# Optimization experiments

Measured on AMD Instinct MI355X. Metric: run time of the kernel, lower is better.

The kernel has to match this reference:

```python
import jax, jax.numpy as jnp
import numpy as np

D = 512
SCALE = 1.0 / np.sqrt(D).astype(np.float32)


def setup_inputs() -> dict:
    key = jax.random.key(0)
    ks = jax.random.split(key, 6)
    B, S = 8, 2048
    x = jax.random.normal(ks[0], (B, S, D), dtype=jnp.float32)
    bias = jax.random.normal(ks[1], (1,), dtype=jnp.float32)
    key_padding_mask = jax.random.randint(ks[2], (B, S), 0, 2).astype(jnp.bool_)
    # nn.Linear weights, stored as [out, in]; y = x @ W.T
    Wq = jax.random.normal(ks[3], (D, D), dtype=jnp.float32) * (1.0 / np.sqrt(D))
    Wk = jax.random.normal(ks[4], (D, D), dtype=jnp.float32) * (1.0 / np.sqrt(D))
    Wv = jax.random.normal(ks[5], (D, D), dtype=jnp.float32) * (1.0 / np.sqrt(D))
    return {"x": x, "bias": bias, "key_padding_mask": key_padding_mask,
            "Wq": Wq, "Wk": Wk, "Wv": Wv}


def reference(x, bias, key_padding_mask, Wq, Wk, Wv):
    # Projections (Linear without bias): [B,S,D] @ [D,D]^T
    Q = jnp.einsum('bsd,ed->bse', x, Wq)
    K = jnp.einsum('bsd,ed->bse', x, Wk)
    V = jnp.einsum('bsd,ed->bse', x, Wv)
    # Scaled scores with additive scalar bias: [B,S,S]
    scores = jnp.einsum('bqd,bkd->bqk', Q, K) * SCALE + bias
    # Key padding mask: mask keys (last dim) with -inf
    scores = jnp.where(key_padding_mask[:, None, :], -jnp.inf, scores)
    attn = jax.nn.softmax(scores, axis=-1)
    attn = jnp.nan_to_num(attn, nan=0.0)  # fully-masked rows -> 0
    # Dropout is inference no-op
    return jnp.einsum('bqk,bkd->bqd', attn, V)
```

## Files before the change

### kernel.cpp

```cpp
#include <hip/hip_runtime.h>

typedef short bf16x8 __attribute__((ext_vector_type(8)));
typedef float f32x4 __attribute__((ext_vector_type(4)));
typedef float f32x16 __attribute__((ext_vector_type(16)));

__device__ __forceinline__ ushort f2bf(float f) {
    union { float f; unsigned u; } v; v.f = f;
    unsigned r = (v.u + 0x7fffu + ((v.u >> 16) & 1u)) >> 16;
    return (ushort)r;
}
__device__ __forceinline__ float bf2f(ushort u) {
    union { unsigned u; float f; } v; v.u = ((unsigned)u) << 16;
    return v.f;
}
__device__ __forceinline__ void async_copy16(void* lds, const void* g) {
    __builtin_amdgcn_global_load_lds(
        (const __attribute__((address_space(1))) unsigned*)g,
        (__attribute__((address_space(3))) unsigned*)lds, 16, 0, 0);
}
__device__ __forceinline__ void lds_barrier() {
    asm volatile("s_waitcnt lgkmcnt(0)\n\ts_barrier" ::: "memory");
}

__global__ __launch_bounds__(256)
void prep_kernel(const float* __restrict__ x, const float* __restrict__ Wq,
                 const float* __restrict__ Wk, const float* __restrict__ Wv,
                 const int* __restrict__ mask,
                 ushort* __restrict__ xb, ushort* __restrict__ wqT,
                 ushort* __restrict__ wkT, ushort* __restrict__ wvb,
                 int* __restrict__ idx, int* __restrict__ cnt)
{
    const int bid = blockIdx.x, t = threadIdx.x;
    if (bid < 8192) {
        int i = (bid * 256 + t) * 4;
        float4 v = *(const float4*)(x + i);
        ushort4 o;
        o.x = f2bf(v.x); o.y = f2bf(v.y); o.z = f2bf(v.z); o.w = f2bf(v.w);
        *(ushort4*)(xb + i) = o;
    } else if (bid < 8320) {
        __shared__ ushort T[64][72];
        int r = bid - 8192;
        const int z = r >> 6; r &= 63;
        const float* in = z ? Wk : Wq;
        ushort* out     = z ? wkT : wqT;
        const int r0 = (r >> 3) * 64, c0 = (r & 7) * 64;
        const int rr = t >> 3, cc8 = (t & 7) * 8;
        #pragma unroll
        for (int pass = 0; pass < 2; ++pass) {
            int rw = rr + pass * 32;
            float4 a = *(const float4*)(in + (size_t)(r0 + rw) * 512 + c0 + cc8);
            float4 bq = *(const float4*)(in + (size_t)(r0 + rw) * 512 + c0 + cc8 + 4);
            T[rw][cc8+0]=f2bf(a.x);  T[rw][cc8+1]=f2bf(a.y);  T[rw][cc8+2]=f2bf(a.z);  T[rw][cc8+3]=f2bf(a.w);
            T[rw][cc8+4]=f2bf(bq.x); T[rw][cc8+5]=f2bf(bq.y); T[rw][cc8+6]=f2bf(bq.z); T[rw][cc8+7]=f2bf(bq.w);
        }
        __syncthreads();
        const int c = t >> 2, seg = (t & 3) * 16;
        ushort tmp[16];
        #pragma unroll
        for (int j = 0; j < 16; ++j) tmp[j] = T[seg + j][c];
        *(uint4*)(out + (size_t)(c0 + c) * 512 + r0 + seg)     = *(uint4*)&tmp[0];
        *(uint4*)(out + (size_t)(c0 + c) * 512 + r0 + seg + 8) = *(uint4*)&tmp[8];
    } else if (bid < 8576) {
        int i = ((bid - 8320) * 256 + t) * 4;
        float4 v = *(const float4*)(Wv + i);
        ushort4 o;
        o.x = f2bf(v.x); o.y = f2bf(v.y); o.z = f2bf(v.z); o.w = f2bf(v.w);
        *(ushort4*)(wvb + i) = o;
    } else {
        __shared__ int sc[256];
        int seg = bid - 8576, b = seg >> 1, half = seg & 1;
        const int* m = mask + b * 2048 + half * 1024;
        int v0 = (m[t*4+0] == 0), v1 = (m[t*4+1] == 0);
        int v2 = (m[t*4+2] == 0), v3 = (m[t*4+3] == 0);
        int c = v0 + v1 + v2 + v3;
        sc[t] = c; __syncthreads();
        for (int ofs = 1; ofs < 256; ofs <<= 1) {
            int xx = (t >= ofs) ? sc[t - ofs] : 0;
            __syncthreads(); sc[t] += xx; __syncthreads();
        }
        int pos = sc[t] - c + seg * 1024;
        if (v0) idx[pos++] = t*4+0;
        if (v1) idx[pos++] = t*4+1;
        if (v2) idx[pos++] = t*4+2;
        if (v3) idx[pos++] = t*4+3;
        if (t == 255) cnt[seg] = sc[255];
    }
}

__device__ __forceinline__ int map_row(const int* __restrict__ idx,
                                       const int* __restrict__ cnt, int row) {
    int seg = row >> 10, j = row & 1023;
    int src = (j < cnt[seg]) ? idx[(seg << 10) + j] : 0;
    return (seg << 10) + src;
}

__device__ __forceinline__ void gemm_core(const ushort* __restrict__ A,
                                          const ushort* __restrict__ B,
                                          ushort* __restrict__ C,
                                          int N, int K, int mBase, int nBase,
                                          int mapA, int mapB,
                                          const int* __restrict__ idx,
                                          const int* __restrict__ cnt)
{
    __shared__ ushort As[128][32];
    __shared__ ushort Bs[128][32];
    const int tid = threadIdx.x;
    const int lane = tid & 63, wave = tid >> 6;
    const int wm = wave >> 1, wn = wave & 1;
    const int lr = lane & 15, lq = lane >> 4;
    const int sr = lane >> 2;
    const int sc = (lane & 3) * 8;

    const ushort* aptr[2];
    const ushort* bptr[2];
    #pragma unroll
    for (int j = 0; j < 2; ++j) {
        int ra = mBase + wave * 32 + j * 16 + sr;
        int rb = nBase + wave * 32 + j * 16 + sr;
        int sa = mapA ? map_row(idx, cnt, ra) : ra;
        int sb = mapB ? map_row(idx, cnt, rb) : rb;
        aptr[j] = A + (size_t)sa * K + sc;
        bptr[j] = B + (size_t)sb * K + sc;
    }

    f32x4 acc[4][4];
    #pragma unroll
    for (int i = 0; i < 4; ++i)
        #pragma unroll
        for (int j = 0; j < 4; ++j) acc[i][j] = (f32x4){0.f, 0.f, 0.f, 0.f};

    for (int k0 = 0; k0 < K; k0 += 32) {
        __syncthreads();
        #pragma unroll
        for (int j = 0; j < 2; ++j) {
            int rbase = wave * 32 + j * 16;
            async_copy16(&As[rbase][0], aptr[j] + k0);
            async_copy16(&Bs[rbase][0], bptr[j] + k0);
        }
        __syncthreads();
        bf16x8 af[4], bfr[4];
        #pragma unroll
        for (int mi = 0; mi < 4; ++mi) af[mi] = *(const bf16x8*)&As[wm * 64 + mi * 16 + lr][lq * 8];
        #pragma unroll
        for (int ni = 0; ni < 4; ++ni) bfr[ni] = *(const bf16x8*)&Bs[wn * 64 + ni * 16 + lr][lq * 8];
        #pragma unroll
        for (int mi = 0; mi < 4; ++mi)
            #pragma unroll
            for (int ni = 0; ni < 4; ++ni)
                acc[mi][ni] = __builtin_amdgcn_mfma_f32_16x16x32_bf16(af[mi], bfr[ni], acc[mi][ni], 0, 0, 0);
    }
    #pragma unroll
    for (int mi = 0; mi < 4; ++mi)
        #pragma unroll
        for (int ni = 0; ni < 4; ++ni)
            #pragma unroll
            for (int r = 0; r < 4; ++r) {
                int m = mBase + wm * 64 + mi * 16 + lq * 4 + r;
                int n = nBase + wn * 64 + ni * 16 + lr;
                C[(size_t)m * N + n] = f2bf(acc[mi][ni][r]);
            }
}

__global__ __launch_bounds__(256, 2)
void gemm_m(const ushort* __restrict__ A, const ushort* __restrict__ B,
            ushort* __restrict__ C) {
    gemm_core(A, B, C, 512, 512, blockIdx.y * 128, blockIdx.x * 128,
              0, 0, nullptr, nullptr);
}

__global__ __launch_bounds__(256, 2)
void gemm_kv(const ushort* __restrict__ xb, const ushort* __restrict__ Mb,
             ushort* __restrict__ Kc, const ushort* __restrict__ wv,
             ushort* __restrict__ Vtc, const int* __restrict__ idx,
             const int* __restrict__ cnt)
{
    if (blockIdx.z == 0) {
        int mBase = blockIdx.y * 128, nBase = blockIdx.x * 128;
        if ((mBase & 1023) >= cnt[mBase >> 10]) return;
        gemm_core(xb, Mb, Kc, 512, 512, mBase, nBase, 1, 0, idx, cnt);
    } else {
        int mBase = blockIdx.x * 128, nBase = blockIdx.y * 128;
        if ((nBase & 1023) >= cnt[nBase >> 10]) return;
        gemm_core(wv, xb, Vtc, 16384, 512, mBase, nBase, 0, 1, idx, cnt);
    }
}

__global__ __launch_bounds__(256, 2)
void attn_kernel(const ushort* __restrict__ Qg, const ushort* __restrict__ Kcg,
                 const ushort* __restrict__ Vtcg, const int* __restrict__ cntg,
                 ushort* __restrict__ Pog, float* __restrict__ Mlg)
{
    const int S = 2048;
    const float SL2E = 0.0637587160f;

    __shared__ ushort Ks[32][548];
    __shared__ ushort Vs[512][36];
    __shared__ ushort Ps[2][32][36];

    const int lin = blockIdx.x + 32 * blockIdx.y + 256 * blockIdx.z;
    const int seg = (lin & 7) * 2 + (lin >> 8);
    const int qt  = (lin >> 3) & 31;
    const int b = seg >> 1, half = seg & 1;

    const int tid = threadIdx.x, lane = tid & 63, wave = tid >> 6;
    const int lr = lane & 15, lq = lane >> 4;
    const int p = wave >> 1, s = wave & 1;
    const int l32 = lane & 31, lh = lane >> 5;

    const int n = cntg[seg];
    const int ntiles = (n + 31) >> 5;

    const ushort* Qp = Qg + ((size_t)b * S + qt * 64 + wave * 16 + lr) * 512;
    bf16x8 qf[16];
    #pragma unroll
    for (int c = 0; c < 16; ++c) qf[c] = *(const bf16x8*)(Qp + c * 32 + lq * 8);

    f32x16 o[8];
    #pragma unroll
    for (int i = 0; i < 8; ++i)
        #pragma unroll
        for (int r = 0; r < 16; ++r) o[i][r] = 0.f;
    float l_i[4] = {0.f, 0.f, 0.f, 0.f};

    const char* Kseg = (const char*)(Kcg + (size_t)seg * 1024 * 512);
    const char* Vseg = (const char*)Vtcg + (size_t)(seg * 1024) * 2;

    {
        #pragma unroll
        for (int i = 0; i < 8; ++i) {
            int row = wave * 8 + i;
            async_copy16(&Ks[row][0], Kseg + (size_t)row * 1024 + lane * 16);
        }
    }

    for (int kt = 0; kt < ntiles; ++kt) {
        const int key0 = kt * 32;
        __syncthreads();
        uint4 vreg[8];
        {
            const char* gV = Vseg + (size_t)key0 * 2;
            #pragma unroll
            for (int i = 0; i < 8; ++i) {
                int off = i * 4096 + tid * 16;
                vreg[i] = *(const uint4*)(gV + (size_t)(off >> 6) * 32768 + (off & 63));
            }
        }
        const bool va0 = (key0 + lr) < n;
        const bool va1 = (key0 + 16 + lr) < n;
        f32x4 sA = (f32x4){0.f,0.f,0.f,0.f}, sB = (f32x4){0.f,0.f,0.f,0.f};
        f32x4 sC = (f32x4){0.f,0.f,0.f,0.f}, sD = (f32x4){0.f,0.f,0.f,0.f};
        __builtin_amdgcn_s_setprio(1);
        #pragma unroll
        for (int ks = 0; ks < 16; ks += 2) {
            bf16x8 kf0a = *(const bf16x8*)&Ks[lr][ks * 32 + lq * 8];
            bf16x8 kf1a = *(const bf16x8*)&Ks[16 + lr][ks * 32 + lq * 8];
            bf16x8 kf0b = *(const bf16x8*)&Ks[lr][(ks + 1) * 32 + lq * 8];
            bf16x8 kf1b = *(const bf16x8*)&Ks[16 + lr][(ks + 1) * 32 + lq * 8];
            sA = __builtin_amdgcn_mfma_f32_16x16x32_bf16(qf[ks], kf0a, sA, 0, 0, 0);
            sB = __builtin_amdgcn_mfma_f32_16x16x32_bf16(qf[ks], kf1a, sB, 0, 0, 0);
            sC = __builtin_amdgcn_mfma_f32_16x16x32_bf16(qf[ks + 1], kf0b, sC, 0, 0, 0);
            sD = __builtin_amdgcn_mfma_f32_16x16x32_bf16(qf[ks + 1], kf1b, sD, 0, 0, 0);
        }
        __builtin_amdgcn_s_setprio(0);
        #pragma unroll
        for (int r = 0; r < 4; ++r) {
            float s0 = sA[r] + sC[r], s1 = sB[r] + sD[r];
            float p0 = va0 ? exp2f(fmaf(s0, SL2E, -8.f)) : 0.f;
            float p1 = va1 ? exp2f(fmaf(s1, SL2E, -8.f)) : 0.f;
            l_i[r] += p0 + p1;
            Ps[p][16 * s + lq * 4 + r][lr]      = f2bf(p0);
            Ps[p][16 * s + lq * 4 + r][16 + lr] = f2bf(p1);
        }
        #pragma unroll
        for (int i = 0; i < 8; ++i) {
            int off = i * 4096 + tid * 16;
            int row = off >> 6, col = off & 63;
            *(uint4*)((char*)Vs + row * 72 + col) = vreg[i];
        }
        lds_barrier();
        if (kt + 1 < ntiles) {
            const char* gK = Kseg + (size_t)(key0 + 32) * 1024;
            #pragma unroll
            for (int i = 0; i < 8; ++i) {
                int row = wave * 8 + i;
                async_copy16(&Ks[row][0], gK + (size_t)row * 1024 + lane * 16);
            }
        }
        bf16x8 pA0 = *(const bf16x8*)&Ps[p][l32][lh * 8];
        bf16x8 pA1 = *(const bf16x8*)&Ps[p][l32][16 + lh * 8];
        __builtin_amdgcn_s_setprio(1);
        #pragma unroll
        for (int dt = 0; dt < 8; ++dt) {
            int d = s * 256 + dt * 32 + l32;
            bf16x8 v0 = *(const bf16x8*)&Vs[d][lh * 8];
            bf16x8 v1 = *(const bf16x8*)&Vs[d][16 + lh * 8];
            o[dt] = __builtin_amdgcn_mfma_f32_32x32x16_bf16(pA0, v0, o[dt], 0, 0, 0);
            o[dt] = __builtin_amdgcn_mfma_f32_32x32x16_bf16(pA1, v1, o[dt], 0, 0, 0);
        }
        __builtin_amdgcn_s_setprio(0);
    }
    #pragma unroll
    for (int r = 0; r < 4; ++r)
        #pragma unroll
        for (int off = 1; off < 16; off <<= 1)
            l_i[r] += __shfl_xor(l_i[r], off, 16);
    const size_t growbase = (size_t)half * 16384 + (size_t)b * S + qt * 64;
    if (lr == 0) {
        #pragma unroll
        for (int r = 0; r < 4; ++r)
            Mlg[growbase + wave * 16 + lq * 4 + r] = l_i[r];
    }
    ushort* Pop = Pog + (growbase + p * 32) * 512;
    #pragma unroll
    for (int dt = 0; dt < 8; ++dt) {
        int ocol = s * 256 + dt * 32 + l32;
        #pragma unroll
        for (int r = 0; r < 16; ++r) {
            int orow = (r & 3) + 8 * (r >> 2) + 4 * lh;
            Pop[(size_t)orow * 512 + ocol] = f2bf(o[dt][r]);
        }
    }
}

__global__ __launch_bounds__(256)
void combine_kernel(const ushort* __restrict__ Po, const float* __restrict__ Ml,
                    float* __restrict__ out)
{
    int i = (blockIdx.x * 256 + threadIdx.x) * 4;
    int row = i >> 9;
    float l = Ml[row] + Ml[16384 + row];
    float s = l > 0.f ? 1.f / l : 0.f;
    ushort4 p1 = *(const ushort4*)(Po + i);
    ushort4 p2 = *(const ushort4*)(Po + 8388608 + i);
    float4 o;
    o.x = (bf2f(p1.x) + bf2f(p2.x)) * s;
    o.y = (bf2f(p1.y) + bf2f(p2.y)) * s;
    o.z = (bf2f(p1.z) + bf2f(p2.z)) * s;
    o.w = (bf2f(p1.w) + bf2f(p2.w)) * s;
    *(float4*)(out + i) = o;
}

extern "C" void kernel_launch(void* const* d_in, const int* in_sizes, int n_in,
                              void* d_out, int out_size, void* d_ws, size_t ws_size,
                              hipStream_t stream) {
    const float* x  = (const float*)d_in[0];
    const int* mask = (const int*)d_in[2];
    const float* Wq = (const float*)d_in[3];
    const float* Wk = (const float*)d_in[4];
    const float* Wv = (const float*)d_in[5];
    float* out = (float*)d_out;

    ushort* ws   = (ushort*)d_ws;
    ushort* xb   = ws;
    ushort* wqT  = ws + 8388608;
    ushort* wkT  = wqT + 262144;
    ushort* wvb  = wkT + 262144;
    ushort* Pob  = ws + 9175040;
    ushort* Mb   = ws + 17563648;
    int*    idxb = (int*)(ws + 17825792);
    ushort* Kc   = ws + 25952256;
    ushort* Vtc  = ws + 34340864;
    float*  Mlb  = (float*)(ws + 42729472);
    int*    cntb = (int*)(ws + 42795008);

    prep_kernel<<<8592, 256, 0, stream>>>(x, Wq, Wk, Wv, mask,
                                          xb, wqT, wkT, wvb, idxb, cntb);
    gemm_m<<<dim3(4, 4), 256, 0, stream>>>(wqT, wkT, Mb);
    gemm_kv<<<dim3(4, 128, 2), 256, 0, stream>>>(xb, Mb, Kc, wvb, Vtc, idxb, cntb);
    attn_kernel<<<dim3(32, 8, 2), 256, 0, stream>>>(xb, Kc, Vtc, cntb, Pob, Mlb);
    combine_kernel<<<8192, 256, 0, stream>>>(Pob, Mlb, out);
}
```

Before: 214.2 us.

## Write V in MFMA-fragment tiled layout and load V directly from global

The V projection epilogue now writes V^T into a layout pre-tiled to match the 32x32x16 MFMA B-operand fragments. The attention kernel then reads V fragments straight from global memory (L2) and drops the Vs LDS staging buffer with its register round-trip. This removes LDS writes and reads for V and frees shared memory, which may allow higher occupancy. In exchange the V loads now sit on the MFMA critical path with global latency, and the K prefetch is issued later in the loop.

```diff
diff --git a/kernel.cpp b/kernel.cpp
--- a/kernel.cpp
+++ b/kernel.cpp
@@ -100,7 +100,8 @@
                                           int N, int K, int mBase, int nBase,
                                           int mapA, int mapB,
                                           const int* __restrict__ idx,
-                                          const int* __restrict__ cnt)
+                                          const int* __restrict__ cnt,
+                                          int vt)
 {
     __shared__ ushort As[128][32];
     __shared__ ushort Bs[128][32];
@@ -157,7 +158,16 @@
             for (int r = 0; r < 4; ++r) {
                 int m = mBase + wm * 64 + mi * 16 + lq * 4 + r;
                 int n = nBase + wn * 64 + ni * 16 + lr;
-                C[(size_t)m * N + n] = f2bf(acc[mi][ni][r]);
+                float val = acc[mi][ni][r];
+                if (!vt) {
+                    C[(size_t)m * N + n] = f2bf(val);
+                } else {
+                    int sseg = n >> 10, key = n & 1023;
+                    size_t ix = (size_t)sseg * 524288 + (size_t)(key >> 5) * 16384
+                              + (size_t)(m >> 5) * 1024 + ((key >> 4) & 1) * 512
+                              + (m & 31) * 16 + (key & 15);
+                    C[ix] = f2bf(val);
+                }
             }
 }
 
@@ -165,7 +175,7 @@
 void gemm_m(const ushort* __restrict__ A, const ushort* __restrict__ B,
             ushort* __restrict__ C) {
     gemm_core(A, B, C, 512, 512, blockIdx.y * 128, blockIdx.x * 128,
-              0, 0, nullptr, nullptr);
+              0, 0, nullptr, nullptr, 0);
 }
 
 __global__ __launch_bounds__(256, 2)
@@ -177,11 +187,11 @@
     if (blockIdx.z == 0) {
         int mBase = blockIdx.y * 128, nBase = blockIdx.x * 128;
         if ((mBase & 1023) >= cnt[mBase >> 10]) return;
-        gemm_core(xb, Mb, Kc, 512, 512, mBase, nBase, 1, 0, idx, cnt);
+        gemm_core(xb, Mb, Kc, 512, 512, mBase, nBase, 1, 0, idx, cnt, 0);
     } else {
         int mBase = blockIdx.x * 128, nBase = blockIdx.y * 128;
         if ((nBase & 1023) >= cnt[nBase >> 10]) return;
-        gemm_core(wv, xb, Vtc, 16384, 512, mBase, nBase, 0, 1, idx, cnt);
+        gemm_core(wv, xb, Vtc, 16384, 512, mBase, nBase, 0, 1, idx, cnt, 1);
     }
 }
 
@@ -194,7 +204,6 @@
     const float SL2E = 0.0637587160f;
 
     __shared__ ushort Ks[32][548];
-    __shared__ ushort Vs[512][36];
     __shared__ ushort Ps[2][32][36];
 
     const int lin = blockIdx.x + 32 * blockIdx.y + 256 * blockIdx.z;
@@ -223,7 +232,7 @@
     float l_i[4] = {0.f, 0.f, 0.f, 0.f};
 
     const char* Kseg = (const char*)(Kcg + (size_t)seg * 1024 * 512);
-    const char* Vseg = (const char*)Vtcg + (size_t)(seg * 1024) * 2;
+    const ushort* Vseg = Vtcg + (size_t)seg * 524288;
 
     {
         #pragma unroll
@@ -236,15 +245,6 @@
     for (int kt = 0; kt < ntiles; ++kt) {
         const int key0 = kt * 32;
         __syncthreads();
-        uint4 vreg[8];
-        {
-            const char* gV = Vseg + (size_t)key0 * 2;
-            #pragma unroll
-            for (int i = 0; i < 8; ++i) {
-                int off = i * 4096 + tid * 16;
-                vreg[i] = *(const uint4*)(gV + (size_t)(off >> 6) * 32768 + (off & 63));
-            }
-        }
         const bool va0 = (key0 + lr) < n;
         const bool va1 = (key0 + 16 + lr) < n;
         f32x4 sA = (f32x4){0.f,0.f,0.f,0.f}, sB = (f32x4){0.f,0.f,0.f,0.f};
@@ -271,13 +271,20 @@
             Ps[p][16 * s + lq * 4 + r][lr]      = f2bf(p0);
             Ps[p][16 * s + lq * 4 + r][16 + lr] = f2bf(p1);
         }
-        #pragma unroll
-        for (int i = 0; i < 8; ++i) {
-            int off = i * 4096 + tid * 16;
-            int row = off >> 6, col = off & 63;
-            *(uint4*)((char*)Vs + row * 72 + col) = vreg[i];
-        }
         lds_barrier();
+        bf16x8 pA0 = *(const bf16x8*)&Ps[p][l32][lh * 8];
+        bf16x8 pA1 = *(const bf16x8*)&Ps[p][l32][16 + lh * 8];
+        const ushort* Vt = Vseg + (size_t)kt * 16384 + l32 * 16 + lh * 8;
+        __builtin_amdgcn_s_setprio(1);
+        #pragma unroll
+        for (int dt = 0; dt < 8; ++dt) {
+            const int db = s * 8 + dt;
+            bf16x8 v0 = *(const bf16x8*)(Vt + db * 1024);
+            bf16x8 v1 = *(const bf16x8*)(Vt + db * 1024 + 512);
+            o[dt] = __builtin_amdgcn_mfma_f32_32x32x16_bf16(pA0, v0, o[dt], 0, 0, 0);
+            o[dt] = __builtin_amdgcn_mfma_f32_32x32x16_bf16(pA1, v1, o[dt], 0, 0, 0);
+        }
+        __builtin_amdgcn_s_setprio(0);
         if (kt + 1 < ntiles) {
             const char* gK = Kseg + (size_t)(key0 + 32) * 1024;
             #pragma unroll
@@ -286,18 +293,6 @@
                 async_copy16(&Ks[row][0], gK + (size_t)row * 1024 + lane * 16);
             }
         }
-        bf16x8 pA0 = *(const bf16x8*)&Ps[p][l32][lh * 8];
-        bf16x8 pA1 = *(const bf16x8*)&Ps[p][l32][16 + lh * 8];
-        __builtin_amdgcn_s_setprio(1);
-        #pragma unroll
-        for (int dt = 0; dt < 8; ++dt) {
-            int d = s * 256 + dt * 32 + l32;
-            bf16x8 v0 = *(const bf16x8*)&Vs[d][lh * 8];
-            bf16x8 v1 = *(const bf16x8*)&Vs[d][16 + lh * 8];
-            o[dt] = __builtin_amdgcn_mfma_f32_32x32x16_bf16(pA0, v0, o[dt], 0, 0, 0);
-            o[dt] = __builtin_amdgcn_mfma_f32_32x32x16_bf16(pA1, v1, o[dt], 0, 0, 0);
-        }
-        __builtin_amdgcn_s_setprio(0);
     }
     #pragma unroll
     for (int r = 0; r < 4; ++r)
```

Result: slower. 250.8 us (+17.1%).

## Fuse Wq^T·Wk product GEMM into prep kernel and widen combine vectors

Applied to the files above, without the earlier changes.

Drops the separate gemm_m launch and the transposed bf16 copies of Wq and Wk. The M = Wq^T·Wk product is now computed inside the prep kernel by 16 extra blocks that read fp32 weights directly, convert to bf16 and transpose into LDS, then run MFMA. This removes one kernel launch and one round-trip of intermediate weight buffers. The combine kernel also switches to 8 elements per thread with 16-byte loads, halving its grid. The trade-off is that these 16 GEMM blocks run inside the large prep grid with uncoalesced scalar LDS stores and no pipelining, so they may become a tail at the end of prep.

```diff
diff --git a/kernel.cpp b/kernel.cpp
--- a/kernel.cpp
+++ b/kernel.cpp
@@ -3,6 +3,7 @@
 typedef short bf16x8 __attribute__((ext_vector_type(8)));
 typedef float f32x4 __attribute__((ext_vector_type(4)));
 typedef float f32x16 __attribute__((ext_vector_type(16)));
+typedef ushort u16x8 __attribute__((ext_vector_type(8)));
 
 __device__ __forceinline__ ushort f2bf(float f) {
     union { float f; unsigned u; } v; v.f = f;
@@ -26,8 +27,8 @@
 void prep_kernel(const float* __restrict__ x, const float* __restrict__ Wq,
                  const float* __restrict__ Wk, const float* __restrict__ Wv,
                  const int* __restrict__ mask,
-                 ushort* __restrict__ xb, ushort* __restrict__ wqT,
-                 ushort* __restrict__ wkT, ushort* __restrict__ wvb,
+                 ushort* __restrict__ xb, ushort* __restrict__ wvb,
+                 ushort* __restrict__ Mb,
                  int* __restrict__ idx, int* __restrict__ cnt)
 {
     const int bid = blockIdx.x, t = threadIdx.x;
@@ -37,38 +38,72 @@
         ushort4 o;
         o.x = f2bf(v.x); o.y = f2bf(v.y); o.z = f2bf(v.z); o.w = f2bf(v.w);
         *(ushort4*)(xb + i) = o;
-    } else if (bid < 8320) {
-        __shared__ ushort T[64][72];
-        int r = bid - 8192;
-        const int z = r >> 6; r &= 63;
-        const float* in = z ? Wk : Wq;
-        ushort* out     = z ? wkT : wqT;
-        const int r0 = (r >> 3) * 64, c0 = (r & 7) * 64;
-        const int rr = t >> 3, cc8 = (t & 7) * 8;
-        #pragma unroll
-        for (int pass = 0; pass < 2; ++pass) {
-            int rw = rr + pass * 32;
-            float4 a = *(const float4*)(in + (size_t)(r0 + rw) * 512 + c0 + cc8);
-            float4 bq = *(const float4*)(in + (size_t)(r0 + rw) * 512 + c0 + cc8 + 4);
-            T[rw][cc8+0]=f2bf(a.x);  T[rw][cc8+1]=f2bf(a.y);  T[rw][cc8+2]=f2bf(a.z);  T[rw][cc8+3]=f2bf(a.w);
-            T[rw][cc8+4]=f2bf(bq.x); T[rw][cc8+5]=f2bf(bq.y); T[rw][cc8+6]=f2bf(bq.z); T[rw][cc8+7]=f2bf(bq.w);
-        }
-        __syncthreads();
-        const int c = t >> 2, seg = (t & 3) * 16;
-        ushort tmp[16];
-        #pragma unroll
-        for (int j = 0; j < 16; ++j) tmp[j] = T[seg + j][c];
-        *(uint4*)(out + (size_t)(c0 + c) * 512 + r0 + seg)     = *(uint4*)&tmp[0];
-        *(uint4*)(out + (size_t)(c0 + c) * 512 + r0 + seg + 8) = *(uint4*)&tmp[8];
-    } else if (bid < 8576) {
-        int i = ((bid - 8320) * 256 + t) * 4;
+    } else if (bid < 8208) {
+        __shared__ ushort As[128][32];
+        __shared__ ushort Bs[128][32];
+        const int bb = bid - 8192;
+        const int m0 = (bb >> 2) * 128, n0 = (bb & 3) * 128;
+        const int lane = t & 63, wave = t >> 6;
+        const int wm = wave >> 1, wn = wave & 1;
+        const int lr = lane & 15, lq = lane >> 4;
+        const int kk = t >> 3, mm = (t & 7) * 16;
+
+        f32x4 acc[4][4];
+        #pragma unroll
+        for (int i2 = 0; i2 < 4; ++i2)
+            #pragma unroll
+            for (int j2 = 0; j2 < 4; ++j2) acc[i2][j2] = (f32x4){0.f,0.f,0.f,0.f};
+
+        for (int k0 = 0; k0 < 512; k0 += 32) {
+            float4 qa[4], kb[4];
+            #pragma unroll
+            for (int j = 0; j < 4; ++j) {
+                qa[j] = *(const float4*)(Wq + (size_t)(k0 + kk) * 512 + m0 + mm + j * 4);
+                kb[j] = *(const float4*)(Wk + (size_t)(k0 + kk) * 512 + n0 + mm + j * 4);
+            }
+            __syncthreads();
+            #pragma unroll
+            for (int j = 0; j < 4; ++j) {
+                As[mm + j*4 + 0][kk] = f2bf(qa[j].x);
+                As[mm + j*4 + 1][kk] = f2bf(qa[j].y);
+                As[mm + j*4 + 2][kk] = f2bf(qa[j].z);
+                As[mm + j*4 + 3][kk] = f2bf(qa[j].w);
+                Bs[mm + j*4 + 0][kk] = f2bf(kb[j].x);
+                Bs[mm + j*4 + 1][kk] = f2bf(kb[j].y);
+                Bs[mm + j*4 + 2][kk] = f2bf(kb[j].z);
+                Bs[mm + j*4 + 3][kk] = f2bf(kb[j].w);
+            }
+            __syncthreads();
+            bf16x8 af[4], bfr[4];
+            #pragma unroll
+            for (int mi = 0; mi < 4; ++mi) af[mi]  = *(const bf16x8*)&As[wm * 64 + mi * 16 + lr][lq * 8];
+            #pragma unroll
+            for (int ni = 0; ni < 4; ++ni) bfr[ni] = *(const bf16x8*)&Bs[wn * 64 + ni * 16 + lr][lq * 8];
+            #pragma unroll
+            for (int mi = 0; mi < 4; ++mi)
+                #pragma unroll
+                for (int ni = 0; ni < 4; ++ni)
+                    acc[mi][ni] = __builtin_amdgcn_mfma_f32_16x16x32_bf16(af[mi], bfr[ni], acc[mi][ni], 0, 0, 0);
+        }
+        #pragma unroll
+        for (int mi = 0; mi < 4; ++mi)
+            #pragma unroll
+            for (int ni = 0; ni < 4; ++ni)
+                #pragma unroll
+                for (int r = 0; r < 4; ++r) {
+                    int m = m0 + wm * 64 + mi * 16 + lq * 4 + r;
+                    int n = n0 + wn * 64 + ni * 16 + lr;
+                    Mb[(size_t)m * 512 + n] = f2bf(acc[mi][ni][r]);
+                }
+    } else if (bid < 8464) {
+        int i = ((bid - 8208) * 256 + t) * 4;
         float4 v = *(const float4*)(Wv + i);
         ushort4 o;
         o.x = f2bf(v.x); o.y = f2bf(v.y); o.z = f2bf(v.z); o.w = f2bf(v.w);
         *(ushort4*)(wvb + i) = o;
     } else {
         __shared__ int sc[256];
-        int seg = bid - 8576, b = seg >> 1, half = seg & 1;
+        int seg = bid - 8464, b = seg >> 1, half = seg & 1;
         const int* m = mask + b * 2048 + half * 1024;
         int v0 = (m[t*4+0] == 0), v1 = (m[t*4+1] == 0);
         int v2 = (m[t*4+2] == 0), v3 = (m[t*4+3] == 0);
@@ -162,13 +197,6 @@
 }
 
 __global__ __launch_bounds__(256, 2)
-void gemm_m(const ushort* __restrict__ A, const ushort* __restrict__ B,
-            ushort* __restrict__ C) {
-    gemm_core(A, B, C, 512, 512, blockIdx.y * 128, blockIdx.x * 128,
-              0, 0, nullptr, nullptr);
-}
-
-__global__ __launch_bounds__(256, 2)
 void gemm_kv(const ushort* __restrict__ xb, const ushort* __restrict__ Mb,
              ushort* __restrict__ Kc, const ushort* __restrict__ wv,
              ushort* __restrict__ Vtc, const int* __restrict__ idx,
@@ -326,18 +354,23 @@
 void combine_kernel(const ushort* __restrict__ Po, const float* __restrict__ Ml,
                     float* __restrict__ out)
 {
-    int i = (blockIdx.x * 256 + threadIdx.x) * 4;
+    int i = (blockIdx.x * 256 + threadIdx.x) * 8;
     int row = i >> 9;
     float l = Ml[row] + Ml[16384 + row];
     float s = l > 0.f ? 1.f / l : 0.f;
-    ushort4 p1 = *(const ushort4*)(Po + i);
-    ushort4 p2 = *(const ushort4*)(Po + 8388608 + i);
-    float4 o;
-    o.x = (bf2f(p1.x) + bf2f(p2.x)) * s;
-    o.y = (bf2f(p1.y) + bf2f(p2.y)) * s;
-    o.z = (bf2f(p1.z) + bf2f(p2.z)) * s;
-    o.w = (bf2f(p1.w) + bf2f(p2.w)) * s;
-    *(float4*)(out + i) = o;
+    u16x8 p1 = *(const u16x8*)(Po + i);
+    u16x8 p2 = *(const u16x8*)(Po + 8388608 + i);
+    float4 o1, o2;
+    o1.x = (bf2f((ushort)p1[0]) + bf2f((ushort)p2[0])) * s;
+    o1.y = (bf2f((ushort)p1[1]) + bf2f((ushort)p2[1])) * s;
+    o1.z = (bf2f((ushort)p1[2]) + bf2f((ushort)p2[2])) * s;
+    o1.w = (bf2f((ushort)p1[3]) + bf2f((ushort)p2[3])) * s;
+    o2.x = (bf2f((ushort)p1[4]) + bf2f((ushort)p2[4])) * s;
+    o2.y = (bf2f((ushort)p1[5]) + bf2f((ushort)p2[5])) * s;
+    o2.z = (bf2f((ushort)p1[6]) + bf2f((ushort)p2[6])) * s;
+    o2.w = (bf2f((ushort)p1[7]) + bf2f((ushort)p2[7])) * s;
+    *(float4*)(out + i)     = o1;
+    *(float4*)(out + i + 4) = o2;
 }
 
 extern "C" void kernel_launch(void* const* d_in, const int* in_sizes, int n_in,
@@ -352,9 +385,7 @@
 
     ushort* ws   = (ushort*)d_ws;
     ushort* xb   = ws;
-    ushort* wqT  = ws + 8388608;
-    ushort* wkT  = wqT + 262144;
-    ushort* wvb  = wkT + 262144;
+    ushort* wvb  = ws + 8912896;
     ushort* Pob  = ws + 9175040;
     ushort* Mb   = ws + 17563648;
     int*    idxb = (int*)(ws + 17825792);
@@ -363,10 +394,9 @@
     float*  Mlb  = (float*)(ws + 42729472);
     int*    cntb = (int*)(ws + 42795008);
 
-    prep_kernel<<<8592, 256, 0, stream>>>(x, Wq, Wk, Wv, mask,
-                                          xb, wqT, wkT, wvb, idxb, cntb);
-    gemm_m<<<dim3(4, 4), 256, 0, stream>>>(wqT, wkT, Mb);
+    prep_kernel<<<8480, 256, 0, stream>>>(x, Wq, Wk, Wv, mask,
+                                          xb, wvb, Mb, idxb, cntb);
     gemm_kv<<<dim3(4, 128, 2), 256, 0, stream>>>(xb, Mb, Kc, wvb, Vtc, idxb, cntb);
     attn_kernel<<<dim3(32, 8, 2), 256, 0, stream>>>(xb, Kc, Vtc, cntb, Pob, Mlb);
-    combine_kernel<<<8192, 256, 0, stream>>>(Pob, Mlb, out);
-}
+    combine_kernel<<<4096, 256, 0, stream>>>(Pob, Mlb, out);
+}
```

Measured after the change: 236.8 us. 10.5% more time.
